# Kernel optimization log

Measured on AMD Instinct MI355X. Metric: run time of the kernel, lower is better.

The kernel has to match this reference:

```python
import jax, jax.numpy as jnp
import numpy as np

B, S, D, DOUT = 4, 4096, 1024, 1024

def setup_inputs() -> dict:
    key = jax.random.key(0)
    k1, k2 = jax.random.split(key)
    x = jax.random.normal(k1, (B, S, D), dtype=jnp.float32)
    kernel = jax.random.normal(k2, (3, D, DOUT), dtype=jnp.float32) * 0.02
    return {"x": x, "kernel": kernel}

def reference(x, kernel):
    # k, q, v: [B, S, DOUT]  (kernel[0]->k, kernel[1]->q, kernel[2]->v as in source)
    k = jnp.einsum('bsd,de->bse', x, kernel[0])
    q = jnp.einsum('bsd,de->bse', x, kernel[1])
    v = jnp.einsum('bsd,de->bse', x, kernel[2])
    dk = jnp.sqrt(jnp.float32(DOUT))
    scores = jnp.einsum('bqe,bke->bqk', q, k) / dk  # [B, S, S]
    weights = jax.nn.softmax(scores, axis=-1)
    return jnp.einsum('bqk,bke->bqe', weights, v)
```

## Files before the change

kernel.cpp:

```cpp
#include <hip/hip_runtime.h>


typedef unsigned short ushort_t;
typedef __attribute__((ext_vector_type(8))) short     bf16x8;
typedef __attribute__((ext_vector_type(4))) float     f32x4;
typedef __attribute__((ext_vector_type(4))) unsigned int u32x4;
typedef __attribute__((ext_vector_type(4))) unsigned short u16x4;

__device__ __forceinline__ unsigned short f2bf(float f) {
  unsigned u = __float_as_uint(f);
  return (unsigned short)((u + 0x7FFFu + ((u >> 16) & 1u)) >> 16);
}
__device__ __forceinline__ float bf2f(unsigned short h) {
  return __uint_as_float((unsigned)h << 16);
}

#define GLOAD16(gsrc, ldst)                                                        \
  __builtin_amdgcn_global_load_lds(                                                \
      (const __attribute__((address_space(1))) void*)(gsrc),                       \
      (__attribute__((address_space(3))) void*)(ldst), 16, 0, 0)
#define WAITVM(N) asm volatile("s_waitcnt vmcnt(" #N ")" ::: "memory")
#define WAITLGKM0() asm volatile("s_waitcnt lgkmcnt(0)" ::: "memory")
#define SCHED0()  __builtin_amdgcn_sched_barrier(0)
#define BARRIER() __builtin_amdgcn_s_barrier()

__global__ __launch_bounds__(256) void cast_bf16_kernel(const float* __restrict__ in,
                                                        ushort_t* __restrict__ out) {
  long i = (long)blockIdx.x * 256 + threadIdx.x;
  const f32x4* p = (const f32x4*)(in + i * 8);
  f32x4 a = p[0], b = p[1];
  u32x4 o;
  o.x = (unsigned)f2bf(a[0]) | ((unsigned)f2bf(a[1]) << 16);
  o.y = (unsigned)f2bf(a[2]) | ((unsigned)f2bf(a[3]) << 16);
  o.z = (unsigned)f2bf(b[0]) | ((unsigned)f2bf(b[1]) << 16);
  o.w = (unsigned)f2bf(b[2]) | ((unsigned)f2bf(b[3]) << 16);
  ((u32x4*)out)[i] = o;
}

__global__ __launch_bounds__(256) void prep_weights_kernel(const float* __restrict__ kern,
                                                           ushort_t* __restrict__ wk,
                                                           ushort_t* __restrict__ wq,
                                                           ushort_t* __restrict__ wvt) {
  int idx = blockIdx.x * 256 + threadIdx.x;
  wk[idx] = f2bf(kern[idx]);
  wq[idx] = f2bf(kern[1048576 + idx] * 0.03125f);
  int e = idx >> 10, d = idx & 1023;
  wvt[idx] = f2bf(kern[2097152 + d * 1024 + e]);
}

template <int OUT_BF16>
__global__ __launch_bounds__(256) void gemm_bt(const ushort_t* __restrict__ A, long lda, long batchA,
                                               const ushort_t* __restrict__ B, long ldb, long batchB,
                                               void* __restrict__ C, long ldc, long batchC,
                                               int K) {
  __shared__ ushort_t lA[128 * 64];
  __shared__ ushort_t lB[128 * 64];

  const int tid  = threadIdx.x;
  const int lane = tid & 63;
  const int wid  = tid >> 6;
  const int wr   = wid >> 1;
  const int wc   = wid & 1;

  const ushort_t* Ab = A + (long)blockIdx.z * batchA + (long)blockIdx.y * 128 * lda;
  const ushort_t* Bb = B + (long)blockIdx.z * batchB + (long)blockIdx.x * 128 * ldb;

  f32x4 acc[4][4] = {};

  const int nkt = K >> 6;
  for (int kt = 0; kt < nkt; ++kt) {
#pragma unroll
    for (int i = 0; i < 4; ++i) {
      int c = tid + i * 256;
      int row = c >> 3, p = c & 7;
      int sc = p ^ (row & 7);
      GLOAD16(Ab + (long)row * lda + kt * 64 + sc * 8, &lA[c * 8]);
    }
#pragma unroll
    for (int i = 0; i < 4; ++i) {
      int c = tid + i * 256;
      int row = c >> 3, p = c & 7;
      int sc = p ^ (row & 7);
      GLOAD16(Bb + (long)row * ldb + kt * 64 + sc * 8, &lB[c * 8]);
    }
    __syncthreads();

    const int lr = lane & 15, lg = lane >> 4;
#pragma unroll
    for (int kk = 0; kk < 2; ++kk) {
      bf16x8 af[4], bfr[4];
#pragma unroll
      for (int m = 0; m < 4; ++m) {
        int row = wr * 64 + m * 16 + lr;
        int cidx = kk * 4 + lg;
        af[m] = *(const bf16x8*)((const char*)lA + row * 128 + ((cidx ^ (row & 7)) << 4));
      }
#pragma unroll
      for (int n = 0; n < 4; ++n) {
        int row = wc * 64 + n * 16 + lr;
        int cidx = kk * 4 + lg;
        bfr[n] = *(const bf16x8*)((const char*)lB + row * 128 + ((cidx ^ (row & 7)) << 4));
      }
#pragma unroll
      for (int m = 0; m < 4; ++m)
#pragma unroll
        for (int n = 0; n < 4; ++n)
          acc[m][n] = __builtin_amdgcn_mfma_f32_16x16x32_bf16(af[m], bfr[n], acc[m][n], 0, 0, 0);
    }
    __syncthreads();
  }

  const long Crow0 = (long)blockIdx.y * 128 + wr * 64;
  const long Ccol0 = (long)blockIdx.x * 128 + wc * 64;
  float*     Cf = (float*)C + (long)blockIdx.z * batchC;
  ushort_t*  Cb = (ushort_t*)C + (long)blockIdx.z * batchC;
#pragma unroll
  for (int m = 0; m < 4; ++m) {
    long r0 = Crow0 + m * 16 + ((lane >> 4) << 2);
#pragma unroll
    for (int n = 0; n < 4; ++n) {
      long cc = Ccol0 + n * 16 + (lane & 15);
#pragma unroll
      for (int j = 0; j < 4; ++j) {
        float val = acc[m][n][j];
        if (OUT_BF16) Cb[(r0 + j) * ldc + cc] = f2bf(val);
        else          Cf[(r0 + j) * ldc + cc] = val;
      }
    }
  }
}

template <int OUT_BF16>
__global__ __launch_bounds__(512, 2) void gemm256(
    const ushort_t* __restrict__ A, long lda, long batchA,
    const ushort_t* __restrict__ B, long ldb, long batchB,
    void* __restrict__ C, long ldc, long batchC,
    int K, int tx, int ty) {
  __shared__ ushort_t lds[2][2][16384];

  const int nb = gridDim.x;
  int f = blockIdx.x;
  f = (f & 7) * (nb >> 3) + (f >> 3);
  const int txy = tx * ty;
  const int bz = f / txy;
  int r = f - bz * txy;
  const int by = r / tx;
  const int bx = r - by * tx;

  const int tid  = threadIdx.x;
  const int lane = tid & 63;
  const int wid  = tid >> 6;
  const int wr   = wid >> 2;
  const int wc   = wid & 3;
  const int lr   = lane & 15, lg = lane >> 4;

  const ushort_t* Ab = A + (long)bz * batchA + (long)by * 256 * lda;
  const ushort_t* Bb = B + (long)bz * batchB + (long)bx * 256 * ldb;

  f32x4 acc[8][4] = {};

  auto stage = [&](int buf, int kt) {
    const ushort_t* As = Ab + (long)kt * 64;
    const ushort_t* Bs = Bb + (long)kt * 64;
#pragma unroll
    for (int i = 0; i < 4; ++i) {
      int c = tid + i * 512;
      int row = c >> 3;
      int sc = (c & 7) ^ (row & 7);
      GLOAD16(As + (long)row * lda + sc * 8, &lds[buf][0][c * 8]);
    }
#pragma unroll
    for (int i = 0; i < 4; ++i) {
      int c = tid + i * 512;
      int row = c >> 3;
      int sc = (c & 7) ^ (row & 7);
      GLOAD16(Bs + (long)row * ldb + sc * 8, &lds[buf][1][c * 8]);
    }
  };

  auto compute = [&](int buf) {
#pragma unroll
    for (int kkt = 0; kkt < 2; ++kkt) {
      bf16x8 a[8], b[4];
#pragma unroll
      for (int m = 0; m < 8; ++m) {
        int row = wr * 128 + m * 16 + lr;
        a[m] = *(const bf16x8*)((const char*)&lds[buf][0][0] + row * 128 +
                                (((kkt * 4 + lg) ^ (row & 7)) << 4));
      }
#pragma unroll
      for (int n = 0; n < 4; ++n) {
        int row = wc * 64 + n * 16 + lr;
        b[n] = *(const bf16x8*)((const char*)&lds[buf][1][0] + row * 128 +
                                (((kkt * 4 + lg) ^ (row & 7)) << 4));
      }
      __builtin_amdgcn_s_setprio(1);
#pragma unroll
      for (int m = 0; m < 8; ++m)
#pragma unroll
        for (int n = 0; n < 4; ++n)
          acc[m][n] = __builtin_amdgcn_mfma_f32_16x16x32_bf16(a[m], b[n], acc[m][n], 0, 0, 0);
      __builtin_amdgcn_s_setprio(0);
    }
  };

  const int nkt = K >> 6;
  stage(0, 0);
  stage(1, 1);
  WAITVM(8);
  BARRIER();
  SCHED0();
  for (int kt = 0; kt < nkt; ++kt) {
    compute(kt & 1);
    WAITLGKM0();
    SCHED0();
    BARRIER();
    SCHED0();
    if (kt + 2 < nkt) {
      stage(kt & 1, kt + 2);
      WAITVM(8);
    } else {
      WAITVM(0);
    }
    BARRIER();
    SCHED0();
  }

  const long Crow0 = (long)by * 256 + wr * 128;
  const long Ccol0 = (long)bx * 256 + wc * 64;
  float*     Cf = (float*)C + (long)bz * batchC;
  ushort_t*  Cb = (ushort_t*)C + (long)bz * batchC;
#pragma unroll
  for (int m = 0; m < 8; ++m) {
    long r0 = Crow0 + m * 16 + ((lane >> 4) << 2);
#pragma unroll
    for (int n = 0; n < 4; ++n) {
      long cc = Ccol0 + n * 16 + (lane & 15);
#pragma unroll
      for (int j = 0; j < 4; ++j) {
        float val = acc[m][n][j];
        if (OUT_BF16) Cb[(r0 + j) * ldc + cc] = f2bf(val);
        else          Cf[(r0 + j) * ldc + cc] = val;
      }
    }
  }
}

__global__ __launch_bounds__(256) void softmax_kernel(float* __restrict__ S,
                                                      ushort_t* __restrict__ P,
                                                      long pstride) {
  float* row = S + (long)blockIdx.x * 4096;
  const int tid = threadIdx.x;
  __shared__ float red[4];

  f32x4 v[4];
#pragma unroll
  for (int i = 0; i < 4; ++i) v[i] = ((const f32x4*)row)[tid + i * 256];

  float m = -1e30f;
#pragma unroll
  for (int i = 0; i < 4; ++i)
#pragma unroll
    for (int j = 0; j < 4; ++j) m = fmaxf(m, v[i][j]);
  for (int o = 32; o; o >>= 1) m = fmaxf(m, __shfl_xor(m, o));
  if ((tid & 63) == 0) red[tid >> 6] = m;
  __syncthreads();
  m = fmaxf(fmaxf(red[0], red[1]), fmaxf(red[2], red[3]));

  float p[16];
  float s = 0.f;
#pragma unroll
  for (int i = 0; i < 4; ++i)
#pragma unroll
    for (int j = 0; j < 4; ++j) {
      float e = __expf(v[i][j] - m);
      p[i * 4 + j] = e;
      s += e;
    }
  for (int o = 32; o; o >>= 1) s += __shfl_xor(s, o);
  __syncthreads();
  if ((tid & 63) == 0) red[tid >> 6] = s;
  __syncthreads();
  s = red[0] + red[1] + red[2] + red[3];
  float inv = 1.0f / s;

  u16x4* prow = (u16x4*)(P + (long)blockIdx.x * pstride);
#pragma unroll
  for (int i = 0; i < 4; ++i) {
    u16x4 o;
    o.x = f2bf(p[i * 4 + 0] * inv);
    o.y = f2bf(p[i * 4 + 1] * inv);
    o.z = f2bf(p[i * 4 + 2] * inv);
    o.w = f2bf(p[i * 4 + 3] * inv);
    prow[tid + i * 256] = o;
  }
}

__global__ __launch_bounds__(256) void softmax_bf16_kernel(ushort_t* __restrict__ S) {
  u16x4* row = (u16x4*)(S + (long)blockIdx.x * 4096);
  const int tid = threadIdx.x;
  __shared__ float red[4];

  float v[16];
#pragma unroll
  for (int i = 0; i < 4; ++i) {
    u16x4 h = row[tid + i * 256];
    v[i * 4 + 0] = bf2f(h.x); v[i * 4 + 1] = bf2f(h.y);
    v[i * 4 + 2] = bf2f(h.z); v[i * 4 + 3] = bf2f(h.w);
  }

  float m = -1e30f;
#pragma unroll
  for (int i = 0; i < 16; ++i) m = fmaxf(m, v[i]);
  for (int o = 32; o; o >>= 1) m = fmaxf(m, __shfl_xor(m, o));
  if ((tid & 63) == 0) red[tid >> 6] = m;
  __syncthreads();
  m = fmaxf(fmaxf(red[0], red[1]), fmaxf(red[2], red[3]));

  float s = 0.f;
#pragma unroll
  for (int i = 0; i < 16; ++i) {
    v[i] = __expf(v[i] - m);
    s += v[i];
  }
  for (int o = 32; o; o >>= 1) s += __shfl_xor(s, o);
  __syncthreads();
  if ((tid & 63) == 0) red[tid >> 6] = s;
  __syncthreads();
  s = red[0] + red[1] + red[2] + red[3];
  float inv = 1.0f / s;

#pragma unroll
  for (int i = 0; i < 4; ++i) {
    u16x4 o;
    o.x = f2bf(v[i * 4 + 0] * inv);
    o.y = f2bf(v[i * 4 + 1] * inv);
    o.z = f2bf(v[i * 4 + 2] * inv);
    o.w = f2bf(v[i * 4 + 3] * inv);
    row[tid + i * 256] = o;
  }
}

extern "C" void kernel_launch(void* const* d_in, const int* in_sizes, int n_in,
                              void* d_out, int out_size, void* d_ws, size_t ws_size,
                              hipStream_t stream) {
  const float* x    = (const float*)d_in[0];
  const float* kern = (const float*)d_in[1];
  float* out = (float*)d_out;

  char* p = (char*)d_ws;
  ushort_t* xbf = (ushort_t*)p; p += 33554432;
  ushort_t* t   = (ushort_t*)p; p += 33554432;
  ushort_t* vT  = (ushort_t*)p; p += 33554432;
  ushort_t* wk  = (ushort_t*)p; p += 2097152;
  ushort_t* wq  = (ushort_t*)p; p += 2097152;
  ushort_t* wvt = (ushort_t*)p; p += 2097152;
  ushort_t* mt  = (ushort_t*)p; p += 2097152;
  size_t fixed = (size_t)(p - (char*)d_ws);

  cast_bf16_kernel<<<8192, 256, 0, stream>>>(x, xbf);
  prep_weights_kernel<<<4096, 256, 0, stream>>>(kern, wk, wq, wvt);
  gemm_bt<1><<<dim3(8, 8, 1), 256, 0, stream>>>(wk, 1024, 0, wq, 1024, 0, mt, 1024, 0, 1024);

  const size_t need4 = fixed + 4ull * 33554432;
  const size_t need2 = fixed + 2ull * 33554432;

  if (ws_size >= need2) {
    ushort_t* Sb = (ushort_t*)p;

    gemm256<1><<<dim3(256), dim3(512), 0, stream>>>(xbf, 1024, 0, mt, 1024, 0,
                                                    t, 1024, 0, 1024, 4, 64);
    gemm256<1><<<dim3(256), dim3(512), 0, stream>>>(wvt, 1024, 0,
                                                    xbf, 1024, 4194304,
                                                    vT, 4096, 4194304, 1024, 16, 4);

    const int nb_at_once = (ws_size >= need4) ? 4 : 2;
    for (int b0 = 0; b0 < 4; b0 += nb_at_once) {
      for (int b = b0; b < b0 + nb_at_once; ++b) {
        gemm256<1><<<dim3(256), dim3(512), 0, stream>>>(
            t + (long)b * 4194304, 1024, 0,
            xbf + (long)b * 4194304, 1024, 0,
            Sb + (long)(b - b0) * 16777216, 4096, 0, 1024, 16, 16);
      }
      softmax_bf16_kernel<<<4096 * nb_at_once, 256, 0, stream>>>(Sb);
      gemm256<0><<<dim3(4 * 16 * nb_at_once), dim3(512), 0, stream>>>(
          Sb, 4096, 16777216,
          vT + (long)b0 * 4194304, 4096, 4194304,
          out + (long)b0 * 4194304, 1024, 4194304, 4096, 4, 16);
    }
  } else {
    float* Sbuf = (float*)p;
    long CR = 4096;
    while (CR > 256 && fixed + (size_t)CR * 4096 * 4 > ws_size) CR >>= 1;

    gemm_bt<1><<<dim3(8, 128, 1), 256, 0, stream>>>(xbf, 1024, 0, mt, 1024, 0, t, 1024, 0, 1024);
    gemm_bt<1><<<dim3(32, 8, 4), 256, 0, stream>>>(wvt, 1024, 0,
                                                   xbf, 1024, 4194304,
                                                   vT, 4096, 4194304, 1024);
    for (int b = 0; b < 4; ++b) {
      const ushort_t* xb  = xbf + (long)b * 4194304;
      const ushort_t* vTb = vT  + (long)b * 4194304;
      for (long c0 = 0; c0 < 4096; c0 += CR) {
        const ushort_t* tb = t + ((long)b * 4096 + c0) * 1024;
        gemm_bt<0><<<dim3(32, CR / 128, 1), 256, 0, stream>>>(tb, 1024, 0, xb, 1024, 0,
                                                              Sbuf, 4096, 0, 1024);
        softmax_kernel<<<CR, 256, 0, stream>>>(Sbuf, (ushort_t*)Sbuf, 8192);
        gemm_bt<0><<<dim3(8, CR / 128, 1), 256, 0, stream>>>((const ushort_t*)Sbuf, 8192, 0,
                                                             vTb, 4096, 0,
                                                             out + ((long)b * 4096 + c0) * 1024, 1024, 0,
                                                             4096);
      }
    }
  }
}
```

Baseline: 428.0 us.

## Split 256-tile GEMM main loop into four interleaved load/MFMA phases

```diff
diff --git a/kernel.cpp b/kernel.cpp
--- a/kernel.cpp
+++ b/kernel.cpp
@@ -130,17 +130,45 @@
   }
 }
 
+
+#define PH0(cb, ob, t1, WN)                         \
+  readA(cb, 0); readB(cb, 0);                       \
+  if (t1 >= 0) { stageA(ob, t1, 1, 0); stageB(ob, t1, 1, 0); } \
+  BARRIER(); WAITVM(WN); WAITLGKM0(); SCHED0();     \
+  mfma16(0, 0);                                     \
+  BARRIER(); SCHED0();
+
+#define PH1(cb, ob, t1, WN)                         \
+  readB(cb, 1);                                     \
+  if (t1 >= 0) { stageA(ob, t1, 1, 1); stageB(ob, t1, 1, 1); } \
+  BARRIER(); WAITVM(WN); WAITLGKM0(); SCHED0();     \
+  mfma16(0, 1);                                     \
+  BARRIER(); SCHED0();
+
+#define PH2(cb, t2, WN)                             \
+  readA(cb, 1);                                     \
+  if (t2 >= 0) { stageA(cb, t2, 0, 0); stageA(cb, t2, 0, 1); } \
+  BARRIER(); WAITVM(WN); WAITLGKM0(); SCHED0();     \
+  mfma16(1, 0);                                     \
+  BARRIER(); SCHED0();
+
+#define PH3(cb, t2, WN)                             \
+  if (t2 >= 0) { stageB(cb, t2, 0, 0); stageB(cb, t2, 0, 1); } \
+  BARRIER(); WAITVM(WN); SCHED0();                  \
+  mfma16(1, 1);                                     \
+  BARRIER(); SCHED0();
+
 template <int OUT_BF16>
-__global__ __launch_bounds__(512, 2) void gemm256(
+__global__ __launch_bounds__(512, 1) void gemm256(
     const ushort_t* __restrict__ A, long lda, long batchA,
     const ushort_t* __restrict__ B, long ldb, long batchB,
     void* __restrict__ C, long ldc, long batchC,
     int K, int tx, int ty) {
   __shared__ ushort_t lds[2][2][16384];
 
-  const int nb = gridDim.x;
+  const int nblk = gridDim.x;
   int f = blockIdx.x;
-  f = (f & 7) * (nb >> 3) + (f >> 3);
+  f = (f & 7) * (nblk >> 3) + (f >> 3);
   const int txy = tx * ty;
   const int bz = f / txy;
   int r = f - bz * txy;
@@ -158,72 +186,87 @@
   const ushort_t* Bb = B + (long)bz * batchB + (long)bx * 256 * ldb;
 
   f32x4 acc[8][4] = {};
-
-  auto stage = [&](int buf, int kt) {
-    const ushort_t* As = Ab + (long)kt * 64;
-    const ushort_t* Bs = Bb + (long)kt * 64;
-#pragma unroll
-    for (int i = 0; i < 4; ++i) {
-      int c = tid + i * 512;
-      int row = c >> 3;
-      int sc = (c & 7) ^ (row & 7);
-      GLOAD16(As + (long)row * lda + sc * 8, &lds[buf][0][c * 8]);
-    }
-#pragma unroll
-    for (int i = 0; i < 4; ++i) {
-      int c = tid + i * 512;
-      int row = c >> 3;
-      int sc = (c & 7) ^ (row & 7);
-      GLOAD16(Bs + (long)row * ldb + sc * 8, &lds[buf][1][c * 8]);
-    }
+  bf16x8 afr[4][2];
+  bf16x8 bfr[4][2];
+
+  auto stageA = [&](int buf, int kt, int alpha, int half) {
+    int c = half * 512 + tid;
+    int r7 = c >> 3;
+    int row = ((r7 & 63) | ((r7 & 64) << 1)) + alpha * 64;
+    int pch = c & 7;
+    int sc = pch ^ (row & 7);
+    GLOAD16(Ab + (long)row * lda + (long)kt * 64 + sc * 8,
+            &lds[buf][0][row * 64 + pch * 8]);
   };
-
-  auto compute = [&](int buf) {
-#pragma unroll
-    for (int kkt = 0; kkt < 2; ++kkt) {
-      bf16x8 a[8], b[4];
-#pragma unroll
-      for (int m = 0; m < 8; ++m) {
-        int row = wr * 128 + m * 16 + lr;
-        a[m] = *(const bf16x8*)((const char*)&lds[buf][0][0] + row * 128 +
-                                (((kkt * 4 + lg) ^ (row & 7)) << 4));
-      }
-#pragma unroll
-      for (int n = 0; n < 4; ++n) {
-        int row = wc * 64 + n * 16 + lr;
-        b[n] = *(const bf16x8*)((const char*)&lds[buf][1][0] + row * 128 +
-                                (((kkt * 4 + lg) ^ (row & 7)) << 4));
-      }
-      __builtin_amdgcn_s_setprio(1);
-#pragma unroll
-      for (int m = 0; m < 8; ++m)
-#pragma unroll
-        for (int n = 0; n < 4; ++n)
-          acc[m][n] = __builtin_amdgcn_mfma_f32_16x16x32_bf16(a[m], b[n], acc[m][n], 0, 0, 0);
-      __builtin_amdgcn_s_setprio(0);
-    }
+  auto stageB = [&](int buf, int kt, int beta, int half) {
+    int c = half * 512 + tid;
+    int r7 = c >> 3;
+    int row = ((r7 & 31) | ((r7 & 96) << 1)) + beta * 32;
+    int pch = c & 7;
+    int sc = pch ^ (row & 7);
+    GLOAD16(Bb + (long)row * ldb + (long)kt * 64 + sc * 8,
+            &lds[buf][1][row * 64 + pch * 8]);
   };
+  auto readA = [&](int buf, int mh) {
+#pragma unroll
+    for (int mm = 0; mm < 4; ++mm)
+#pragma unroll
+      for (int kk = 0; kk < 2; ++kk) {
+        int row = wr * 128 + (mh * 4 + mm) * 16 + lr;
+        afr[mm][kk] = *(const bf16x8*)((const char*)&lds[buf][0][0] + row * 128 +
+                                       (((kk * 4 + lg) ^ (row & 7)) << 4));
+      }
+  };
+  auto readB = [&](int buf, int nh) {
+#pragma unroll
+    for (int nn = 0; nn < 2; ++nn)
+#pragma unroll
+      for (int kk = 0; kk < 2; ++kk) {
+        int row = wc * 64 + (nh * 2 + nn) * 16 + lr;
+        bfr[nh * 2 + nn][kk] = *(const bf16x8*)((const char*)&lds[buf][1][0] + row * 128 +
+                                                (((kk * 4 + lg) ^ (row & 7)) << 4));
+      }
+  };
+  auto mfma16 = [&](int mh, int nh) {
+    __builtin_amdgcn_s_setprio(1);
+#pragma unroll
+    for (int kk = 0; kk < 2; ++kk)
+#pragma unroll
+      for (int mm = 0; mm < 4; ++mm)
+#pragma unroll
+        for (int nn = 0; nn < 2; ++nn)
+          acc[mh * 4 + mm][nh * 2 + nn] = __builtin_amdgcn_mfma_f32_16x16x32_bf16(
+              afr[mm][kk], bfr[nh * 2 + nn][kk], acc[mh * 4 + mm][nh * 2 + nn], 0, 0, 0);
+    __builtin_amdgcn_s_setprio(0);
+  };
 
   const int nkt = K >> 6;
-  stage(0, 0);
-  stage(1, 1);
-  WAITVM(8);
-  BARRIER();
-  SCHED0();
-  for (int kt = 0; kt < nkt; ++kt) {
-    compute(kt & 1);
-    WAITLGKM0();
-    SCHED0();
-    BARRIER();
-    SCHED0();
-    if (kt + 2 < nkt) {
-      stage(kt & 1, kt + 2);
-      WAITVM(8);
-    } else {
-      WAITVM(0);
-    }
-    BARRIER();
-    SCHED0();
+  stageA(0, 0, 0, 0); stageA(0, 0, 0, 1); stageB(0, 0, 0, 0); stageB(0, 0, 0, 1);
+  stageA(0, 0, 1, 0); stageA(0, 0, 1, 1); stageB(0, 0, 1, 0); stageB(0, 0, 1, 1);
+  stageA(1, 1, 0, 0); stageA(1, 1, 0, 1); stageB(1, 1, 0, 0); stageB(1, 1, 0, 1);
+  WAITVM(4);
+  BARRIER(); SCHED0();
+
+  for (int t = 0; t < nkt - 2; ++t) {
+    const int cb = t & 1, ob = cb ^ 1;
+    PH0(cb, ob, t + 1, 6)
+    PH1(cb, ob, t + 1, 6)
+    PH2(cb, t + 2, 6)
+    PH3(cb, t + 2, 6)
+  }
+  {
+    const int t = nkt - 2, cb = t & 1, ob = cb ^ 1;
+    PH0(cb, ob, t + 1, 6)
+    PH1(cb, ob, t + 1, 6)
+    PH2(cb, -1, 6)
+    PH3(cb, -1, 4)
+  }
+  {
+    const int cb = (nkt - 1) & 1, ob = cb ^ 1;
+    PH0(cb, ob, -1, 0)
+    PH1(cb, ob, -1, 0)
+    PH2(cb, -1, 0)
+    PH3(cb, -1, 0)
   }
 
   const long Crow0 = (long)by * 256 + wr * 128;
```

New measurement: 412.2 us. 1.04x faster.
